# Performance work log

Hardware: AMD Instinct MI355X
Metric: run time of the kernel (lower is better)

Reference implementation:

```python
import math
import jax, jax.numpy as jnp
import numpy as np

B, N, D_MODEL, H = 2, 4096, 2048, 16
HEAD_DIM = D_MODEL // H
CHUNK = 128  # chunk length for the lightning-attention recurrence


def _slopes(n_heads):
    # ALiBi-style slopes used by lightning attention (n_heads is a power of 2)
    start = 2.0 ** (-(2.0 ** -(math.log2(n_heads) - 3)))
    return np.array([start ** (i + 1) for i in range(n_heads)], dtype=np.float32)


def setup_inputs() -> dict:
    key = jax.random.key(0)
    kx, k1, k2, k3, k4 = jax.random.split(key, 5)
    scale = 1.0 / math.sqrt(D_MODEL)
    x = jax.random.normal(kx, (B, N, D_MODEL), dtype=jnp.float32)
    w_qkv = jax.random.normal(k1, (3 * D_MODEL, D_MODEL), dtype=jnp.float32) * scale
    b_qkv = jax.random.normal(k2, (3 * D_MODEL,), dtype=jnp.float32) * 0.01
    w_out = jax.random.normal(k3, (D_MODEL, D_MODEL), dtype=jnp.float32) * scale
    b_out = jax.random.normal(k4, (D_MODEL,), dtype=jnp.float32) * 0.01
    return {"x": x, "w_qkv": w_qkv, "b_qkv": b_qkv, "w_out": w_out, "b_out": b_out}


def _lightning_attn(q, k, v):
    # q,k,v: (B, H, N, d). Causal linear attention with per-head decay lam:
    #   S_t = lam * S_{t-1} + k_t v_t^T ;  o_t = q_t S_t
    b, h, n, d = q.shape
    nc = n // CHUNK
    lam = jnp.exp(-jnp.asarray(_slopes(h)))  # (H,)

    pos = jnp.arange(CHUNK, dtype=jnp.float32)
    decay_q = lam[:, None] ** (pos + 1.0)            # (H, C) inter-chunk q scaling
    decay_k = lam[:, None] ** (CHUNK - 1.0 - pos)    # (H, C) state-update k scaling
    diff = pos[:, None] - pos[None, :]
    causal = diff >= 0
    dmask = jnp.where(causal, lam[:, None, None] ** jnp.maximum(diff, 0.0), 0.0)  # (H,C,C)
    lam_c = lam ** CHUNK                              # (H,)

    def to_chunks(t):
        return t.reshape(b, h, nc, CHUNK, d).transpose(2, 0, 1, 3, 4)  # (nc,B,H,C,d)

    qc, kc, vc = to_chunks(q), to_chunks(k), to_chunks(v)

    def step(S, inp):
        qb, kb, vb = inp  # each (B,H,C,d); S: (B,H,d,d)
        inter = jnp.einsum('bhcd,bhde->bhce', qb * decay_q[None, :, :, None], S)
        scores = jnp.einsum('bhcd,bhed->bhce', qb, kb) * dmask[None]
        intra = jnp.einsum('bhce,bhed->bhcd', scores, vb)
        S_new = lam_c[None, :, None, None] * S + jnp.einsum(
            'bhcd,bhce->bhde', kb * decay_k[None, :, :, None], vb)
        return S_new, inter + intra

    S0 = jnp.zeros((b, h, d, d), dtype=q.dtype)
    _, out = jax.lax.scan(step, S0, (qc, kc, vc))  # out: (nc,B,H,C,d)
    return out.transpose(1, 2, 0, 3, 4).reshape(b, h, n, d)


def reference(x, w_qkv, b_qkv, w_out, b_out):
    b, n, dm = x.shape
    qkv = x @ w_qkv.T + b_qkv                         # (B,N,3D)
    q, k, v = jnp.split(qkv, 3, axis=-1)
    def heads(t):
        return t.reshape(b, n, H, HEAD_DIM).transpose(0, 2, 1, 3)  # (B,H,N,d)
    attn = _lightning_attn(heads(q), heads(k), heads(v))
    attn = attn.transpose(0, 2, 1, 3).reshape(b, n, dm)
    return attn @ w_out.T + b_out
```

## Files before the change

kernel.cpp:

```cpp
#include <hip/hip_runtime.h>
#include <stdint.h>

#define DM    2048
#define NSEQ  4096
#define BB    2
#define NH    16
#define HD    128
#define CHK   128
#define NCHK  32
#define NBH   (BB*NH)
#define MTOT  (BB*NSEQ)
#define N3    (3*DM)

typedef unsigned short u16;
typedef unsigned int   u32;
typedef __attribute__((ext_vector_type(8))) short s16x8;
typedef __attribute__((ext_vector_type(4))) short s16x4;
typedef __attribute__((ext_vector_type(4))) float f32x4;
typedef __attribute__((ext_vector_type(2))) unsigned short u16x2;

__device__ __forceinline__ float b2f(u16 b){ u32 u = ((u32)b) << 16; float f; __builtin_memcpy(&f,&u,4); return f; }
__device__ __forceinline__ u16 f2b(float f){ u32 u; __builtin_memcpy(&u,&f,4); u += 0x7fffu + ((u>>16)&1u); return (u16)(u>>16); }

__device__ __forceinline__ void gload16(const u16* g, u16* l){
  __builtin_amdgcn_global_load_lds((const __attribute__((address_space(1))) void*)g,
                                   (__attribute__((address_space(3))) void*)l, 16, 0, 0);
}

__global__ __launch_bounds__(256) void conv_bf16(const float* __restrict__ src,
                                                 u16* __restrict__ dst, int n4)
{
  for (int i = blockIdx.x*blockDim.x + threadIdx.x; i < n4; i += gridDim.x*blockDim.x){
    f32x4 v = *(const f32x4*)(src + (size_t)i*4);
    s16x4 o;
    #pragma unroll
    for (int j=0;j<4;j++) o[j] = (short)f2b(v[j]);
    *(s16x4*)(dst + (size_t)i*4) = o;
  }
}


#define GEMM256_CORE(GA_, GB_)                                                  \
  __shared__ u16 lds[65536];                                       \
  const int tid  = threadIdx.x;                                                 \
  const int lane = tid & 63;                                                    \
  const int w    = tid >> 6;                                                    \
  const int wm_i = w >> 2, wn_i = w & 3;                                        \
  const int m0 = blockIdx.y << 8;                                               \
  const int n0 = blockIdx.x << 8;                                               \
  const int l15 = lane & 15, lg = lane >> 4, l7 = lane & 7;                     \
  const int c0 = ((lg)     ^ l7) << 3;          \
  const int c1 = ((4 + lg) ^ l7) << 3;                      \
  const int abase = wm_i*8192 + l15*64;                                         \
  const int bbase = 32768 + (wn_i>>1)*8192 + (wn_i&1)*4096 + l15*64;            \
  const int grow = lane >> 3;                                                   \
  const int gcol = ((lane & 7) ^ grow) * 8;                                     \
  const u16* gAl = GA_ + (size_t)(m0 + grow)*DM + gcol;                         \
  const u16* gBl = GB_ + (size_t)(n0 + grow)*DM + gcol;                         \
  auto STG = [&](const u16* gl, int ldsbase, int h, int kt){                    \
    _Pragma("unroll")                                                           \
    for (int j=0;j<2;j++)                                                       \
      gload16(gl + ((size_t)(h*128 + j*64 + w*8))*DM + (size_t)kt*64,           \
              lds + ldsbase + (j*64 + w*8)*64);                                 \
  };                                                                            \
  f32x4 acc[8][4];                                                              \
  _Pragma("unroll")                                                             \
  for (int m=0;m<8;m++)                                                         \
    _Pragma("unroll")                                                           \
    for (int n=0;n<4;n++) acc[m][n] = f32x4{0.f,0.f,0.f,0.f};                   \
  s16x8 bfr[4][2];                                                              \
           \
  STG(gBl, 32768,             0, 0); STG(gBl, 32768+8192,       1, 0);          \
  STG(gAl, 0,                 0, 0); STG(gAl, 8192,             1, 0);          \
  STG(gBl, 32768+16384,       0, 1); STG(gBl, 32768+16384+8192, 1, 1);          \
  asm volatile("s_waitcnt vmcnt(4)" ::: "memory");                              \
  __builtin_amdgcn_s_barrier();                                                 \
  for (int it=0; it<15; ++it){                                                  \
    const int k1 = 2*it+1, k2 = 2*it+2, k3 = 2*it+3;                            \
    PH(0,0,0,1, STG(gAl, 16384,             0, k1), (void)0);                   \
    PH(0,1,0,1, STG(gAl, 16384+8192,        1, k1), (void)0);                   \
    PH(0,0,4,0, STG(gBl, 32768,             0, k2), (void)0);                   \
    PH(0,1,4,0, STG(gBl, 32768+8192,        1, k2),                             \
            asm volatile("s_waitcnt vmcnt(4)" ::: "memory"));                   \
    PH(1,0,0,1, STG(gAl, 0,                 0, k2), (void)0);                   \
    PH(1,1,0,1, STG(gAl, 8192,              1, k2), (void)0);                   \
    PH(1,0,4,0, STG(gBl, 32768+16384,       0, k3), (void)0);                   \
    PH(1,1,4,0, STG(gBl, 32768+16384+8192,  1, k3),                             \
            asm volatile("s_waitcnt vmcnt(4)" ::: "memory"));                   \
  }                                                                             \
                      \
  PH(0,0,0,1, STG(gAl, 16384,      0, 31), (void)0);                            \
  PH(0,1,0,1, STG(gAl, 16384+8192, 1, 31), (void)0);                            \
  PH(0,0,4,0, (void)0, (void)0);                                                \
  PH(0,1,4,0, (void)0, asm volatile("s_waitcnt vmcnt(0)" ::: "memory"));        \
  PH(1,0,0,1, (void)0, (void)0); PH(1,1,0,1, (void)0, (void)0);                 \
  PH(1,0,4,0, (void)0, (void)0); PH(1,1,4,0, (void)0, (void)0);

#define PH(D, KK, MB, BFRD, STAGE, VM) do{                                      \
  s16x8 af[4];                                                                  \
  const int cc_ = (KK) ? c1 : c0;                                               \
  if (BFRD){                                                                    \
    _Pragma("unroll")                                                           \
    for (int n=0;n<4;n++)                                                       \
      bfr[n][KK] = *(const s16x8*)(lds + bbase + (D)*16384 + n*1024 + cc_);     \
  }                                                                             \
  _Pragma("unroll")                                                             \
  for (int j=0;j<4;j++)                                                         \
    af[j] = *(const s16x8*)(lds + abase + (D)*16384 + ((MB)+j)*1024 + cc_);     \
  STAGE;                                                                        \
  VM;                                                                           \
  __builtin_amdgcn_s_barrier();                                                 \
  __builtin_amdgcn_s_setprio(1);                                                \
  _Pragma("unroll")                                                             \
  for (int j=0;j<4;j++)                                                         \
    _Pragma("unroll")                                                           \
    for (int n=0;n<4;n++)                                                       \
      acc[(MB)+j][n] = __builtin_amdgcn_mfma_f32_16x16x32_bf16(                 \
          af[j], bfr[n][KK], acc[(MB)+j][n], 0,0,0);                            \
  __builtin_amdgcn_s_setprio(0);                                                \
}while(0)

__global__ __launch_bounds__(512, 2) void gemm_qkv(const u16* __restrict__ Xb,
    const u16* __restrict__ Wb, const float* __restrict__ bias,
    u16* __restrict__ Qb, u16* __restrict__ Kb, u16* __restrict__ Vb)
{
  GEMM256_CORE(Xb, Wb)

  #pragma unroll
  for (int n=0;n<4;n++){
    const int gn = n0 + wn_i*64 + n*16 + l15;
    const float bv = bias[gn];
    const int which = gn >> 11;
    const int h = (gn >> 7) & 15;
    const int e = gn & 127;
    u16* base_ = (which==0) ? Qb : ((which==1) ? Kb : Vb);
    #pragma unroll
    for (int m=0;m<8;m++){
      #pragma unroll
      for (int r=0;r<4;r++){
        const int gm = m0 + wm_i*128 + m*16 + lg*4 + r;
        const int b  = gm >> 12;
        const int tt = gm & (NSEQ-1);
        base_[(((size_t)(b*NH + h))*NSEQ + tt)*HD + e] = f2b(acc[m][n][r] + bv);
      }
    }
  }
}

__global__ __launch_bounds__(512, 2) void gemm_out(const u16* __restrict__ Ab,
    const u16* __restrict__ Wb, const float* __restrict__ bias,
    float* __restrict__ Out)
{
  GEMM256_CORE(Ab, Wb)

  #pragma unroll
  for (int n=0;n<4;n++){
    const int gn = n0 + wn_i*64 + n*16 + l15;
    const float bv = bias[gn];
    #pragma unroll
    for (int m=0;m<8;m++){
      #pragma unroll
      for (int r=0;r<4;r++){
        const int gm = m0 + wm_i*128 + m*16 + lg*4 + r;
        Out[(size_t)gm*DM + gn] = acc[m][n][r] + bv;
      }
    }
  }
}

__global__ __launch_bounds__(256) void chunk_kv(const u16* __restrict__ Kb,
    const u16* __restrict__ Vb, u16* __restrict__ USb)
{
  __shared__ short Kt[128][152];
  __shared__ short Vt[128][152];
  __shared__ float dkt[128];
  const int tid = threadIdx.x;
  const int blk = blockIdx.x;
  const int c  = blk & (NCHK-1);
  const int bh = blk >> 5;
  const int h  = bh & (NH-1);
  const float slope = exp2f(-0.5f*(float)(h+1));

  if (tid < 128) dkt[tid] = expf(-slope*(float)(CHK-1-tid));
  __syncthreads();

  const u16* kg = Kb + ((size_t)bh*NSEQ + (size_t)c*CHK)*HD;
  const u16* vg = Vb + ((size_t)bh*NSEQ + (size_t)c*CHK)*HD;

  const int e0 = (tid & 63) * 2;
  const int tq = tid >> 6;
  #pragma unroll
  for (int it=0; it<4; it++){
    const int tb = it*32 + tq*8;
    s16x8 k0v, k1v, v0v, v1v;
    #pragma unroll
    for (int j=0;j<8;j++){
      const int t = tb + j;
      u16x2 kv = *(const u16x2*)(kg + (size_t)t*HD + e0);
      u16x2 vv = *(const u16x2*)(vg + (size_t)t*HD + e0);
      const float dk = dkt[t];
      k0v[j] = (short)f2b(b2f(kv[0])*dk);
      k1v[j] = (short)f2b(b2f(kv[1])*dk);
      v0v[j] = (short)vv[0];
      v1v[j] = (short)vv[1];
    }
    *(s16x8*)&Kt[e0  ][tb] = k0v;
    *(s16x8*)&Kt[e0+1][tb] = k1v;
    *(s16x8*)&Vt[e0  ][tb] = v0v;
    *(s16x8*)&Vt[e0+1][tb] = v1v;
  }
  __syncthreads();

  const int lane = tid & 63;
  const int l15 = lane & 15, lg = lane >> 4;
  const int w = tid >> 6;
  const int wm = (w >> 1) << 6, wn = (w & 1) << 6;
  f32x4 acc[4][4];
  #pragma unroll
  for (int i=0;i<4;i++)
    #pragma unroll
    for (int j=0;j<4;j++) acc[i][j] = f32x4{0.f,0.f,0.f,0.f};

  #pragma unroll
  for (int ks=0; ks<4; ks++){
    const int kk = ks*32 + lg*8;
    s16x8 af[4], bf[4];
    #pragma unroll
    for (int m=0;m<4;m++) af[m] = *(const s16x8*)&Kt[wm + m*16 + l15][kk];
    #pragma unroll
    for (int n=0;n<4;n++) bf[n] = *(const s16x8*)&Vt[wn + n*16 + l15][kk];
    #pragma unroll
    for (int m=0;m<4;m++)
      #pragma unroll
      for (int n=0;n<4;n++)
        acc[m][n] = __builtin_amdgcn_mfma_f32_16x16x32_bf16(af[m], bf[n], acc[m][n], 0,0,0);
  }

  u16* up = USb + (size_t)blk*(HD*HD);
  #pragma unroll
  for (int m=0;m<4;m++)
    #pragma unroll
    for (int n=0;n<4;n++)
      #pragma unroll
      for (int r=0;r<4;r++){
        const int d = wm + m*16 + lg*4 + r;
        const int f = wn + n*16 + l15;
        up[d*HD + f] = f2b(acc[m][n][r]);
      }
}

__global__ __launch_bounds__(256) void scan_state(u16* __restrict__ USb)
{
  const int bh = blockIdx.x >> 3;
  const int rs = blockIdx.x & 7;
  const int tid = threadIdx.x;
  const int h = bh & (NH-1);
  const float slope = exp2f(-0.5f*(float)(h+1));
  const float lamC = expf(-slope*(float)CHK);
  float s[8];
  #pragma unroll
  for (int i=0;i<8;i++) s[i]=0.f;
  u16* base = USb + (size_t)bh*NCHK*HD*HD + rs*2048;
  const int off = tid*8;
  for (int c=0;c<NCHK;c++){
    u16* p = base + (size_t)c*HD*HD + off;
    s16x8 u = *(const s16x8*)p;
    s16x8 wv;
    #pragma unroll
    for (int j=0;j<8;j++) wv[j] = (short)f2b(s[j]);
    *(s16x8*)p = wv;
    #pragma unroll
    for (int j=0;j<8;j++) s[j] = lamC*s[j] + b2f((u16)u[j]);
  }
}

__global__ __launch_bounds__(512) void attn_chunk(
    const u16* __restrict__ Qb, const u16* __restrict__ Kb, const u16* __restrict__ Vb,
    const u16* __restrict__ Sb, u16* __restrict__ ATT)
{
  __shared__ short alds[73728];
  __shared__ float qtab[132];
  short* Qs = alds;
  short* Ks = alds + 17408;
  short* Vt = alds + 34816;
  short* St = alds + 54272;

  const int tid = threadIdx.x;
  const int blk = blockIdx.x;
  const int c  = blk & (NCHK-1);
  const int bh = blk >> 5;
  const int b  = bh >> 4, h = bh & 15;
  const float slope = exp2f(-0.5f*(float)(h+1));

  if (tid < 129) qtab[tid] = expf(-slope*(float)tid);

  const size_t qoff = ((size_t)bh*NSEQ + (size_t)c*CHK)*HD;

  #pragma unroll
  for (int i=0;i<4;i++){
    const int lin = i*4096 + tid*8;
    const int r = lin >> 7, e = lin & 127;
    *(s16x8*)&Qs[r*136 + e] = *(const s16x8*)(Qb + qoff + lin);
    *(s16x8*)&Ks[r*136 + e] = *(const s16x8*)(Kb + qoff + lin);
  }
  {
    const int f0 = (tid & 63)*2;
    const int tq = tid >> 6;
    const u16* vg = Vb + qoff;
    const u16* sg = Sb + ((size_t)bh*NCHK + c)*HD*HD;
    #pragma unroll
    for (int it=0; it<2; it++){
      const int t0 = it*64 + tq*8;
      s16x8 v0v, v1v, s0v, s1v;
      #pragma unroll
      for (int j=0;j<8;j++){
        u16x2 v2 = *(const u16x2*)(vg + (size_t)(t0+j)*HD + f0);
        u16x2 s2 = *(const u16x2*)(sg + (size_t)(t0+j)*HD + f0);
        v0v[j]=(short)v2[0]; v1v[j]=(short)v2[1];
        s0v[j]=(short)s2[0]; s1v[j]=(short)s2[1];
      }
      *(s16x8*)&Vt[(f0  )*152 + t0] = v0v;
      *(s16x8*)&Vt[(f0+1)*152 + t0] = v1v;
      *(s16x8*)&St[(f0  )*152 + t0] = s0v;
      *(s16x8*)&St[(f0+1)*152 + t0] = s1v;
    }
  }
  __syncthreads();

  const int lane = tid & 63;
  const int l15 = lane & 15, lg = lane >> 4;
  const int w = tid >> 6;
  const int wrow = (w >> 1) << 5;
  const int wcol = (w & 1) << 6;

  f32x4 accs[2][4], acco[2][4];
  #pragma unroll
  for (int m=0;m<2;m++)
    #pragma unroll
    for (int n=0;n<4;n++){ accs[m][n]=f32x4{0.f,0.f,0.f,0.f}; acco[m][n]=f32x4{0.f,0.f,0.f,0.f}; }

  #pragma unroll
  for (int ks=0; ks<4; ks++){
    const int kk = ks*32 + lg*8;
    s16x8 qa[2], kb_[4], sb_[4];
    #pragma unroll
    for (int m=0;m<2;m++) qa[m] = *(const s16x8*)&Qs[(wrow + m*16 + l15)*136 + kk];
    #pragma unroll
    for (int n=0;n<4;n++){
      kb_[n] = *(const s16x8*)&Ks[(wcol + n*16 + l15)*136 + kk];
      sb_[n] = *(const s16x8*)&St[(wcol + n*16 + l15)*152 + kk];
    }
    #pragma unroll
    for (int m=0;m<2;m++)
      #pragma unroll
      for (int n=0;n<4;n++){
        accs[m][n] = __builtin_amdgcn_mfma_f32_16x16x32_bf16(qa[m], kb_[n], accs[m][n], 0,0,0);
        acco[m][n] = __builtin_amdgcn_mfma_f32_16x16x32_bf16(qa[m], sb_[n], acco[m][n], 0,0,0);
      }
  }
  __syncthreads();

  #pragma unroll
  for (int m=0;m<2;m++){
    #pragma unroll
    for (int r=0;r<4;r++){
      const int t = wrow + m*16 + lg*4 + r;
      const float dq = qtab[t+1];
      #pragma unroll
      for (int n=0;n<4;n++){
        const int s = wcol + n*16 + l15;
        float v = accs[m][n][r];
        v = (t >= s) ? v*qtab[t-s] : 0.f;
        Ks[t*136 + s] = (short)f2b(v);
        acco[m][n][r] *= dq;
      }
    }
  }
  __syncthreads();

  #pragma unroll
  for (int ks=0; ks<4; ks++){
    const int kk = ks*32 + lg*8;
    s16x8 sa[2], vb_[4];
    #pragma unroll
    for (int m=0;m<2;m++) sa[m] = *(const s16x8*)&Ks[(wrow + m*16 + l15)*136 + kk];
    #pragma unroll
    for (int n=0;n<4;n++) vb_[n] = *(const s16x8*)&Vt[(wcol + n*16 + l15)*152 + kk];
    #pragma unroll
    for (int m=0;m<2;m++)
      #pragma unroll
      for (int n=0;n<4;n++)
        acco[m][n] = __builtin_amdgcn_mfma_f32_16x16x32_bf16(sa[m], vb_[n], acco[m][n], 0,0,0);
  }

  u16* op = ATT + ((size_t)(b*NSEQ + c*CHK))*DM + h*HD;
  #pragma unroll
  for (int m=0;m<2;m++)
    #pragma unroll
    for (int n=0;n<4;n++)
      #pragma unroll
      for (int r=0;r<4;r++){
        const int t = wrow + m*16 + lg*4 + r;
        const int f = wcol + n*16 + l15;
        op[(size_t)t*DM + f] = f2b(acco[m][n][r]);
      }
}

extern "C" void kernel_launch(void* const* d_in, const int* in_sizes, int n_in,
                              void* d_out, int out_size, void* d_ws, size_t ws_size,
                              hipStream_t stream)
{
  const float* x     = (const float*)d_in[0];
  const float* w_qkv = (const float*)d_in[1];
  const float* b_qkv = (const float*)d_in[2];
  const float* w_out = (const float*)d_in[3];
  const float* b_out = (const float*)d_in[4];
  float* out = (float*)d_out;

  char* ws = (char*)d_ws;
  const size_t SZ = (size_t)MTOT * DM * sizeof(u16);
  u16* Qb    = (u16*)(ws);
  u16* Kb    = (u16*)(ws + SZ);
  u16* Vb    = (u16*)(ws + 2*SZ);
  u16* USb   = (u16*)(ws + 3*SZ);
  u16* ATT   = (u16*)(ws + 4*SZ);
  u16* Xb    = ATT;
  u16* Wqkvb = USb;
  u16* Woutb = Kb;

  conv_bf16 <<<dim3(2048), 256, 0, stream>>>(x,     Xb,    MTOT*DM/4);
  conv_bf16 <<<dim3(2048), 256, 0, stream>>>(w_qkv, Wqkvb, N3*DM/4);
  gemm_qkv  <<<dim3(N3/256,  MTOT/256), 512, 0, stream>>>(Xb, Wqkvb, b_qkv, Qb, Kb, Vb);
  chunk_kv  <<<dim3(NBH*NCHK),          256, 0, stream>>>(Kb, Vb, USb);
  scan_state<<<dim3(NBH*8),             256, 0, stream>>>(USb);
  attn_chunk<<<dim3(NBH*NCHK),          512, 0, stream>>>(Qb, Kb, Vb, USb, ATT);
  conv_bf16 <<<dim3(1024), 256, 0, stream>>>(w_out, Woutb, DM*DM/4);
  gemm_out  <<<dim3(DM/256,  MTOT/256), 512, 0, stream>>>(ATT, Woutb, b_out, out);
}
```

Measured before the change: 361.0 us.

## Store chunk state transposed and merge the two fp32-to-bf16 conversion launches

The chunk_kv kernel now writes each per-chunk KV state transposed (f-major), by swapping its MFMA operands. This lets attn_chunk load the state with contiguous 16-byte vector copies into LDS instead of doing a strided 2-element gather and transpose. Separately, the x and w_qkv conversions are merged into one grid-stride kernel, which removes one launch. The scan over states is elementwise, so it is unaffected by the layout change, but the producer and consumer must stay consistent.

```diff
diff --git a/kernel.cpp b/kernel.cpp
--- a/kernel.cpp
+++ b/kernel.cpp
@@ -25,6 +25,23 @@
 __device__ __forceinline__ void gload16(const u16* g, u16* l){
   __builtin_amdgcn_global_load_lds((const __attribute__((address_space(1))) void*)g,
                                    (__attribute__((address_space(3))) void*)l, 16, 0, 0);
+}
+
+__global__ __launch_bounds__(256) void conv_all(const float* __restrict__ x,
+    u16* __restrict__ xb, const float* __restrict__ wq, u16* __restrict__ wqb)
+{
+  const int n1 = MTOT*DM/4;
+  const int n2 = N3*DM/4;
+  for (int i = blockIdx.x*blockDim.x + threadIdx.x; i < n1+n2; i += gridDim.x*blockDim.x){
+    const float* s; u16* d; int k;
+    if (i < n1){ s = x;  d = xb;  k = i; }
+    else       { s = wq; d = wqb; k = i - n1; }
+    f32x4 v = *(const f32x4*)(s + (size_t)k*4);
+    s16x4 o;
+    #pragma unroll
+    for (int j=0;j<4;j++) o[j] = (short)f2b(v[j]);
+    *(s16x4*)(d + (size_t)k*4) = o;
+  }
 }
 
 __global__ __launch_bounds__(256) void conv_bf16(const float* __restrict__ src,
@@ -226,9 +243,9 @@
     const int kk = ks*32 + lg*8;
     s16x8 af[4], bf[4];
     #pragma unroll
-    for (int m=0;m<4;m++) af[m] = *(const s16x8*)&Kt[wm + m*16 + l15][kk];
-    #pragma unroll
-    for (int n=0;n<4;n++) bf[n] = *(const s16x8*)&Vt[wn + n*16 + l15][kk];
+    for (int m=0;m<4;m++) af[m] = *(const s16x8*)&Vt[wm + m*16 + l15][kk];
+    #pragma unroll
+    for (int n=0;n<4;n++) bf[n] = *(const s16x8*)&Kt[wn + n*16 + l15][kk];
     #pragma unroll
     for (int m=0;m<4;m++)
       #pragma unroll
@@ -243,9 +260,9 @@
     for (int n=0;n<4;n++)
       #pragma unroll
       for (int r=0;r<4;r++){
-        const int d = wm + m*16 + lg*4 + r;
-        const int f = wn + n*16 + l15;
-        up[d*HD + f] = f2b(acc[m][n][r]);
+        const int f = wm + m*16 + lg*4 + r;
+        const int d = wn + n*16 + l15;
+        up[f*HD + d] = f2b(acc[m][n][r]);
       }
 }
 
@@ -295,6 +312,7 @@
   if (tid < 129) qtab[tid] = expf(-slope*(float)tid);
 
   const size_t qoff = ((size_t)bh*NSEQ + (size_t)c*CHK)*HD;
+  const u16* sg = Sb + ((size_t)bh*NCHK + c)*HD*HD;
 
   #pragma unroll
   for (int i=0;i<4;i++){
@@ -302,27 +320,23 @@
     const int r = lin >> 7, e = lin & 127;
     *(s16x8*)&Qs[r*136 + e] = *(const s16x8*)(Qb + qoff + lin);
     *(s16x8*)&Ks[r*136 + e] = *(const s16x8*)(Kb + qoff + lin);
+    *(s16x8*)&St[r*136 + e] = *(const s16x8*)(sg + lin);
   }
   {
     const int f0 = (tid & 63)*2;
     const int tq = tid >> 6;
     const u16* vg = Vb + qoff;
-    const u16* sg = Sb + ((size_t)bh*NCHK + c)*HD*HD;
     #pragma unroll
     for (int it=0; it<2; it++){
       const int t0 = it*64 + tq*8;
-      s16x8 v0v, v1v, s0v, s1v;
+      s16x8 v0v, v1v;
       #pragma unroll
       for (int j=0;j<8;j++){
         u16x2 v2 = *(const u16x2*)(vg + (size_t)(t0+j)*HD + f0);
-        u16x2 s2 = *(const u16x2*)(sg + (size_t)(t0+j)*HD + f0);
         v0v[j]=(short)v2[0]; v1v[j]=(short)v2[1];
-        s0v[j]=(short)s2[0]; s1v[j]=(short)s2[1];
       }
       *(s16x8*)&Vt[(f0  )*152 + t0] = v0v;
       *(s16x8*)&Vt[(f0+1)*152 + t0] = v1v;
-      *(s16x8*)&St[(f0  )*152 + t0] = s0v;
-      *(s16x8*)&St[(f0+1)*152 + t0] = s1v;
     }
   }
   __syncthreads();
@@ -348,7 +362,7 @@
     #pragma unroll
     for (int n=0;n<4;n++){
       kb_[n] = *(const s16x8*)&Ks[(wcol + n*16 + l15)*136 + kk];
-      sb_[n] = *(const s16x8*)&St[(wcol + n*16 + l15)*152 + kk];
+      sb_[n] = *(const s16x8*)&St[(wcol + n*16 + l15)*136 + kk];
     }
     #pragma unroll
     for (int m=0;m<2;m++)
@@ -428,8 +442,7 @@
   u16* Wqkvb = USb;
   u16* Woutb = Kb;
 
-  conv_bf16 <<<dim3(2048), 256, 0, stream>>>(x,     Xb,    MTOT*DM/4);
-  conv_bf16 <<<dim3(2048), 256, 0, stream>>>(w_qkv, Wqkvb, N3*DM/4);
+  conv_all  <<<dim3(2048), 256, 0, stream>>>(x, Xb, w_qkv, Wqkvb);
   gemm_qkv  <<<dim3(N3/256,  MTOT/256), 512, 0, stream>>>(Xb, Wqkvb, b_qkv, Qb, Kb, Vb);
   chunk_kv  <<<dim3(NBH*NCHK),          256, 0, stream>>>(Kb, Vb, USb);
   scan_state<<<dim3(NBH*8),             256, 0, stream>>>(USb);
```

Measured after the change: 359.7 us. About the same (-0.4%).
